# Performance work log

Hardware: AMD Instinct MI355X
Metric: run time of the kernel (lower is better)

## Reference

```python
import jax, jax.numpy as jnp
import numpy as np
from functools import partial

VOCAB, D, H, L, T_MAX = 32000, 1024, 16, 8, 1024
HD = D // H
HIDDEN = int(D * 2.67)  # 2734, matches int(n_embd*hidden_mult)


def setup_inputs() -> dict:
    key = jax.random.key(0)
    ks = jax.random.split(key, 9)
    s = 0.02
    return {
        "idx": jax.random.randint(ks[0], (2, 1024), 0, VOCAB),
        "W_emb": jax.random.normal(ks[1], (VOCAB, D), jnp.float32) * s,  # tied with lm_head
        "norm1_w": jnp.ones((L, D), jnp.float32),
        "Wqkv": jax.random.normal(ks[2], (L, D, 3 * D), jnp.float32) * s,
        "Wout": jax.random.normal(ks[3], (L, D, D), jnp.float32) * s,
        "norm2_w": jnp.ones((L, D), jnp.float32),
        "Wg": jax.random.normal(ks[4], (L, D, HIDDEN), jnp.float32) * s,
        "Wu": jax.random.normal(ks[5], (L, D, HIDDEN), jnp.float32) * s,
        "Wd": jax.random.normal(ks[6], (L, HIDDEN, D), jnp.float32) * s,
        "final_norm_w": jnp.ones((D,), jnp.float32),
    }


def _rmsnorm(x, w, eps=1e-6):
    rms = jnp.sqrt(jnp.mean(x * x, axis=-1, keepdims=True) + eps)
    return x / rms * w


def _rope(x, cos_f, sin_f):
    # x: [B,H,T,hd]; cos_f/sin_f: [T, hd//2]
    x1, x2 = x[..., : HD // 2], x[..., HD // 2 :]
    c = cos_f[None, None]
    s = sin_f[None, None]
    return jnp.concatenate([x1 * c - x2 * s, x1 * s + x2 * c], axis=-1)


def _forward(idx, W_emb, norm1_w, Wqkv, Wout, norm2_w, Wg, Wu, Wd, final_norm_w):
    B, T = idx.shape
    # RoPE tables (buffers in the torch module)
    inv_freq = 1.0 / (10000.0 ** (jnp.arange(0, HD, 2, dtype=jnp.float32) / HD))
    ang = jnp.arange(T, dtype=jnp.float32)[:, None] * inv_freq[None, :]  # [T, hd//2]
    cos_f, sin_f = jnp.cos(ang), jnp.sin(ang)
    causal = jnp.tril(jnp.ones((T, T), dtype=bool))  # [T,T]
    scale = 1.0 / jnp.sqrt(jnp.float32(HD))

    def block(x, params):
        n1, wqkv, wout, n2, wg, wu, wd = params
        h = _rmsnorm(x, n1)
        qkv = (h @ wqkv).reshape(B, T, 3, H, HD).transpose(2, 0, 3, 1, 4)  # [3,B,H,T,hd]
        q, k, v = qkv[0], qkv[1], qkv[2]
        q = _rope(q, cos_f, sin_f)
        k = _rope(k, cos_f, sin_f)
        attn = jnp.einsum("bhqd,bhkd->bhqk", q, k) * scale
        attn = jnp.where(causal[None, None], attn, -jnp.inf)
        attn = jax.nn.softmax(attn, axis=-1)
        o = jnp.einsum("bhqk,bhkd->bhqd", attn, v)
        o = o.transpose(0, 2, 1, 3).reshape(B, T, D) @ wout
        x = x + o
        h2 = _rmsnorm(x, n2)
        x = x + (jax.nn.silu(h2 @ wg) * (h2 @ wu)) @ wd
        return x, None

    x = W_emb[idx]  # [B,T,D]
    x, _ = jax.lax.scan(block, x, (norm1_w, Wqkv, Wout, norm2_w, Wg, Wu, Wd))
    x = _rmsnorm(x, final_norm_w)
    return x @ W_emb.T  # tied lm_head -> [B,T,VOCAB]


def reference(idx, W_emb, norm1_w, Wqkv, Wout, norm2_w, Wg, Wu, Wd, final_norm_w):
    return _forward(idx, W_emb, norm1_w, Wqkv, Wout, norm2_w, Wg, Wu, Wd, final_norm_w)
```

## Files before the change

kernel.cpp:

```cpp
#include <hip/hip_runtime.h>
#include <cstdint>
#include <cmath>

#define D_MODEL 1024
#define T_SEQ   1024
#define NHEAD   16
#define NLAYER  8
#define HID     2734
#define HID_PAD 2816
#define NTOK    2048
#define VOCAB   32000

typedef __bf16 bf16x8 __attribute__((ext_vector_type(8)));
typedef __bf16 bf16x4 __attribute__((ext_vector_type(4)));
typedef float  f32x4  __attribute__((ext_vector_type(4)));

__device__ inline bf16x4 to_bf4(float a, float b, float c, float d) {
  bf16x4 t; t[0] = (__bf16)a; t[1] = (__bf16)b; t[2] = (__bf16)c; t[3] = (__bf16)d; return t;
}

__device__ inline void gload16(const __bf16* g, __bf16* l) {
  __builtin_amdgcn_global_load_lds(
      (const __attribute__((address_space(1))) void*)g,
      (__attribute__((address_space(3))) void*)l, 16, 0, 0);
}

__global__ __launch_bounds__(256) void embed_kernel(const int* __restrict__ idx,
                                                    const float* __restrict__ W,
                                                    float* __restrict__ x) {
  int t = blockIdx.x;
  int v = idx[t];
  float4 val = *(const float4*)&W[(size_t)v * D_MODEL + threadIdx.x * 4];
  *(float4*)&x[(size_t)t * D_MODEL + threadIdx.x * 4] = val;
}

__global__ __launch_bounds__(256) void rmsnorm_kernel(const float* __restrict__ x,
                                                      const float* __restrict__ w,
                                                      __bf16* __restrict__ out) {
  int row = blockIdx.x;
  int tid = threadIdx.x;
  float4 v = *(const float4*)&x[(size_t)row * D_MODEL + tid * 4];
  float s = v.x * v.x + v.y * v.y + v.z * v.z + v.w * v.w;
#pragma unroll
  for (int m = 32; m >= 1; m >>= 1) s += __shfl_xor(s, m, 64);
  __shared__ float red[4];
  if ((tid & 63) == 0) red[tid >> 6] = s;
  __syncthreads();
  float tot = red[0] + red[1] + red[2] + red[3];
  float inv = rsqrtf(tot * (1.0f / (float)D_MODEL) + 1e-6f);
  float4 wv = *(const float4*)&w[tid * 4];
  bf16x4 o4 = to_bf4(v.x * inv * wv.x, v.y * inv * wv.y, v.z * inv * wv.z, v.w * inv * wv.w);
  *(bf16x4*)&out[(size_t)row * D_MODEL + tid * 4] = o4;
}

__global__ __launch_bounds__(256) void rope_table_kernel(float* __restrict__ tab) {
  int p = blockIdx.x * 256 + threadIdx.x;
  int t = p >> 5, i = p & 31;
  float freq = exp2f(-(float)i * (13.287712379549449f / 32.0f));
  float sn, cs;
  sincosf((float)t * freq, &sn, &cs);
  tab[p] = cs;
  tab[32768 + p] = sn;
}

__global__ __launch_bounds__(256) void tp5_kernel(
    const float* __restrict__ Wqkv, const float* __restrict__ Wout,
    const float* __restrict__ Wg, const float* __restrict__ Wu,
    const float* __restrict__ Wd,
    __bf16* __restrict__ wqkvT, __bf16* __restrict__ woutT,
    __bf16* __restrict__ wguT, __bf16* __restrict__ wdT) {
  __shared__ __bf16 tile[64][65];
  int t = blockIdx.x;
  const float* in;
  __bf16* out;
  int R, C, Ro, rmul, roff, tr;
  if (t < 768)        { in = Wqkv; out = wqkvT; R = 1024; C = 3072; Ro = 1024; rmul = 1; roff = 0; tr = 16; }
  else if (t < 1024)  { t -= 768;  in = Wout; out = woutT; R = 1024; C = 1024; Ro = 1024; rmul = 1; roff = 0; tr = 16; }
  else if (t < 1728)  { t -= 1024; in = Wg; out = wguT; R = 1024; C = HID; Ro = 1024; rmul = 2; roff = 0; tr = 16; }
  else if (t < 2432)  { t -= 1728; in = Wu; out = wguT; R = 1024; C = HID; Ro = 1024; rmul = 2; roff = 1; tr = 16; }
  else                { t -= 2432; in = Wd; out = wdT; R = HID; C = 1024; Ro = HID_PAD; rmul = 1; roff = 0; tr = 44; }
  int r0 = (t % tr) * 64, c0 = (t / tr) * 64;
  int tid = threadIdx.x;
  bool fullc = (c0 + 64 <= C);
#pragma unroll
  for (int i = 0; i < 4; ++i) {
    int ri = i * 16 + (tid >> 4);
    int ci = (tid & 15) * 4;
    int r = r0 + ri;
    float4 v = {0.f, 0.f, 0.f, 0.f};
    if (r < R) {
      const float* p = in + (size_t)r * C + c0 + ci;
      if (fullc) {
        v = *(const float4*)p;
      } else {
        int c = c0 + ci;
        if (c + 0 < C) v.x = p[0];
        if (c + 1 < C) v.y = p[1];
        if (c + 2 < C) v.z = p[2];
        if (c + 3 < C) v.w = p[3];
      }
    }
    tile[ri][ci + 0] = (__bf16)v.x;
    tile[ri][ci + 1] = (__bf16)v.y;
    tile[ri][ci + 2] = (__bf16)v.z;
    tile[ri][ci + 3] = (__bf16)v.w;
  }
  __syncthreads();
#pragma unroll
  for (int i = 0; i < 4; ++i) {
    int oc = i * 16 + (tid >> 4);
    int orr = (tid & 15) * 4;
    bf16x4 tv;
    tv[0] = tile[orr + 0][oc];
    tv[1] = tile[orr + 1][oc];
    tv[2] = tile[orr + 2][oc];
    tv[3] = tile[orr + 3][oc];
    *(bf16x4*)&out[((size_t)(c0 + oc) * rmul + roff) * Ro + r0 + orr] = tv;
  }
}

__global__ __launch_bounds__(256) void convert_bf16_kernel(const float* __restrict__ in,
                                                           __bf16* __restrict__ out, int n4) {
  for (int i = blockIdx.x * 256 + threadIdx.x; i < n4; i += gridDim.x * 256) {
    float4 v = ((const float4*)in)[i];
    ((bf16x4*)out)[i] = to_bf4(v.x, v.y, v.z, v.w);
  }
}

template <int BM, int BN, int WM, int WN, int EPI>
__global__ __launch_bounds__(WM * WN * 64, 2) void gemm8(
    const __bf16* __restrict__ A, const __bf16* __restrict__ B,
    const float* __restrict__ Cin, void* __restrict__ Cout,
    int K, int ldc,
    const float* __restrict__ Tab, __bf16* __restrict__ Qr,
    __bf16* __restrict__ Kr, __bf16* __restrict__ Vt) {
  constexpr int NTH = WM * WN * 64;
  constexpr int MF = BM / (16 * WM);
  constexpr int MG = (MF + 3) / 4;
  constexpr int CL = (MF < 4) ? MF : 4;
  constexpr int LA = (BM * 4) / NTH;
  constexpr int LB = (BN * 4) / NTH;
  static_assert(BN / WN == 64, "NF must be 4");
  __shared__ __align__(16) __bf16 lds[(BM + BN) * 128];

  const int tid = threadIdx.x;
  const int lane = tid & 63, wid = tid >> 6;
  const int wr = wid / WN, wn = wid % WN;
  const int lr = lane & 15, lg = lane >> 4;

  const int gx = gridDim.x;
  const int nwg = gx * gridDim.y;
  const int orig = blockIdx.y * gx + blockIdx.x;
  const int q = nwg >> 3, r8 = nwg & 7;
  const int xcd = orig & 7, loc = orig >> 3;
  const int swz = ((xcd < r8) ? xcd * (q + 1) : r8 * (q + 1) + (xcd - r8) * q) + loc;
  const int brow = (swz % gx) * BM;
  const int bcol = (swz / gx) * BN;

  const __bf16* pAg[LA];
  const __bf16* pBg[LB];
  int opA[LA], opB[LB];
#pragma unroll
  for (int i = 0; i < LA; ++i) {
    int p = tid + i * NTH;
    int row = ((p >> 6) << 4) | (p & 15), j = (p >> 4) & 3;
    pAg[i] = A + (size_t)(brow + row) * K + j * 8;
    opA[i] = p * 8;
  }
#pragma unroll
  for (int i = 0; i < LB; ++i) {
    int p = tid + i * NTH;
    int row = ((p >> 6) << 4) | (p & 15), j = (p >> 4) & 3;
    pBg[i] = B + (size_t)(bcol + row) * K + j * 8;
    opB[i] = p * 8;
  }

  const int ntiles = K >> 6;

  auto STAGE_A = [&](int v, int kkq) {
    int vs = v < ntiles ? v : ntiles - 1;
    int ko = vs * 64 + kkq * 32;
    int sa = (v & 1) * (BM * 64) + kkq * (BM * 32);
#pragma unroll
    for (int i = 0; i < LA; ++i) gload16(pAg[i] + ko, lds + sa + opA[i]);
  };
  auto STAGE_B = [&](int v, int kkq) {
    int vs = v < ntiles ? v : ntiles - 1;
    int ko = vs * 64 + kkq * 32;
    int sb = BM * 128 + (v & 1) * (BN * 64) + kkq * (BN * 32);
#pragma unroll
    for (int i = 0; i < LB; ++i) gload16(pBg[i] + ko, lds + sb + opB[i]);
  };

  f32x4 acc[MF][4];
#pragma unroll
  for (int m = 0; m < MF; ++m)
#pragma unroll
    for (int n = 0; n < 4; ++n) acc[m][n] = (f32x4){0.f, 0.f, 0.f, 0.f};

  STAGE_A(0, 0); STAGE_B(0, 0);
  STAGE_A(0, 1); STAGE_B(0, 1);
  STAGE_A(1, 0); STAGE_B(1, 0);

  const int fragoff = lg * 128 + lr * 8;

  if constexpr (MF == 8) {
    for (int u = 0; u < ntiles; ++u) {
      const int buf = u & 1;
#pragma unroll
      for (int kk = 0; kk < 2; ++kk) {
        const int v = (kk == 0) ? u + 1 : u + 2;
        const int kkq = kk ^ 1;
        const __bf16* Ab = lds + buf * (BM * 64) + kk * (BM * 32);
        const __bf16* Bb = lds + BM * 128 + buf * (BN * 64) + kk * (BN * 32);
        asm volatile("s_waitcnt vmcnt(8)" ::: "memory");
        __builtin_amdgcn_sched_barrier(0);
        __builtin_amdgcn_s_barrier();
        __builtin_amdgcn_sched_barrier(0);
        STAGE_A(v, kkq);
        bf16x8 bfr[4], af0[4];
#pragma unroll
        for (int n = 0; n < 4; ++n)
          bfr[n] = *(const bf16x8*)(Bb + (wn * 64 + n * 16) * 32 + fragoff);
#pragma unroll
        for (int i = 0; i < 4; ++i)
          af0[i] = *(const bf16x8*)(Ab + (wr * 128 + i * 16) * 32 + fragoff);
        asm volatile("s_waitcnt lgkmcnt(0)" ::: "memory");
        __builtin_amdgcn_sched_barrier(0);
        __builtin_amdgcn_s_setprio(1);
#pragma unroll
        for (int i = 0; i < 4; ++i)
#pragma unroll
          for (int n = 0; n < 4; ++n)
            acc[i][n] = __builtin_amdgcn_mfma_f32_16x16x32_bf16(af0[i], bfr[n], acc[i][n], 0, 0, 0);
        __builtin_amdgcn_s_setprio(0);
        __builtin_amdgcn_s_barrier();
        STAGE_B(v, kkq);
        bf16x8 af1[4];
#pragma unroll
        for (int i = 0; i < 4; ++i)
          af1[i] = *(const bf16x8*)(Ab + (wr * 128 + 64 + i * 16) * 32 + fragoff);
        asm volatile("s_waitcnt lgkmcnt(0)" ::: "memory");
        __builtin_amdgcn_sched_barrier(0);
        __builtin_amdgcn_s_setprio(1);
#pragma unroll
        for (int i = 0; i < 4; ++i)
#pragma unroll
          for (int n = 0; n < 4; ++n)
            acc[4 + i][n] = __builtin_amdgcn_mfma_f32_16x16x32_bf16(af1[i], bfr[n], acc[4 + i][n], 0, 0, 0);
        __builtin_amdgcn_s_setprio(0);
        __builtin_amdgcn_s_barrier();
      }
    }
  } else {
    for (int u = 0; u < ntiles; ++u) {
      const int buf = u & 1;
#pragma unroll
      for (int kk = 0; kk < 2; ++kk) {
        if constexpr (LA + LB == 3) asm volatile("s_waitcnt vmcnt(6)" ::: "memory");
        else                        asm volatile("s_waitcnt vmcnt(8)" ::: "memory");
        __builtin_amdgcn_sched_barrier(0);
        __builtin_amdgcn_s_barrier();
        __builtin_amdgcn_sched_barrier(0);
        const int v = (kk == 0) ? u + 1 : u + 2;
        const int kkq = kk ^ 1;
        STAGE_A(v, kkq);
        STAGE_B(v, kkq);
        const __bf16* Ab = lds + buf * (BM * 64) + kk * (BM * 32);
        const __bf16* Bb = lds + BM * 128 + buf * (BN * 64) + kk * (BN * 32);
        bf16x8 bfr[4];
#pragma unroll
        for (int n = 0; n < 4; ++n)
          bfr[n] = *(const bf16x8*)(Bb + (wn * 64 + n * 16) * 32 + fragoff);
#pragma unroll
        for (int mg = 0; mg < MG; ++mg) {
          bf16x8 afr[CL];
#pragma unroll
          for (int i = 0; i < CL; ++i)
            afr[i] = *(const bf16x8*)(Ab + (wr * (BM / WM) + (mg * 4 + i) * 16) * 32 + fragoff);
          __builtin_amdgcn_s_setprio(1);
#pragma unroll
          for (int i = 0; i < CL; ++i)
#pragma unroll
            for (int n = 0; n < 4; ++n)
              acc[mg * 4 + i][n] =
                  __builtin_amdgcn_mfma_f32_16x16x32_bf16(afr[i], bfr[n], acc[mg * 4 + i][n], 0, 0, 0);
          __builtin_amdgcn_s_setprio(0);
        }
      }
    }
  }

  if constexpr (EPI == 5) {
    const int colw = bcol + wn * 64;
    const int secw = colw >> 10;
    const int h = (colw >> 6) & 15;
#pragma unroll
    for (int m = 0; m < MF; ++m) {
      int row0 = brow + wr * (BM / WM) + m * 16 + lg * 4;
      int bb = row0 >> 10;
      int t0 = row0 & 1023;
      int bh = bb * 16 + h;
      if (secw < 2) {
        __bf16* base = (secw == 0 ? Qr : Kr) + ((size_t)bh * T_SEQ + t0) * 64;
#pragma unroll
        for (int n = 0; n < 2; ++n) {
          int din = n * 16 + lr;
#pragma unroll
          for (int rr = 0; rr < 4; ++rr) {
            float a = acc[m][n][rr], b2 = acc[m][n + 2][rr];
            float cs = Tab[(t0 + rr) * 32 + din];
            float sn = Tab[32768 + (t0 + rr) * 32 + din];
            base[(size_t)rr * 64 + din]      = (__bf16)(a * cs - b2 * sn);
            base[(size_t)rr * 64 + din + 32] = (__bf16)(a * sn + b2 * cs);
          }
        }
      } else {
#pragma unroll
        for (int n = 0; n < 4; ++n) {
          int din = n * 16 + lr;
          bf16x4 pk;
#pragma unroll
          for (int rr = 0; rr < 4; ++rr) pk[rr] = (__bf16)acc[m][n][rr];
          *(bf16x4*)&Vt[((size_t)bh * 64 + din) * T_SEQ + t0] = pk;
        }
      }
    }
  } else {
#pragma unroll
    for (int m = 0; m < MF; ++m) {
#pragma unroll
      for (int n = 0; n < 4; ++n) {
#pragma unroll
        for (int rr = 0; rr < 4; ++rr) {
          int row = brow + wr * (BM / WM) + m * 16 + lg * 4 + rr;
          int col = bcol + wn * 64 + n * 16 + lr;
          size_t off = (size_t)row * ldc + col;
          float vv = acc[m][n][rr];
          if (EPI == 0) {
            ((float*)Cout)[off] = vv;
          } else if (EPI == 1) {
            ((float*)Cout)[off] = Cin[off] + vv;
          } else {
            float uv = __shfl_xor(vv, 1);
            if ((lr & 1) == 0) {
              float r = vv / (1.f + __expf(-vv)) * uv;
              ((__bf16*)Cout)[(size_t)row * ldc + (col >> 1)] = (__bf16)r;
            }
          }
        }
      }
    }
  }
}

__global__ __launch_bounds__(256) void attn_kernel(const __bf16* __restrict__ Qr,
                                                   const __bf16* __restrict__ Kr,
                                                   const __bf16* __restrict__ Vt,
                                                   __bf16* __restrict__ o) {
  __shared__ __align__(16) __bf16 lds[28672];
  const int tid = threadIdx.x;
  const int lane = tid & 63, w = tid >> 6;
  const int lr = lane & 15, lg = lane >> 4;
  const int bh = blockIdx.y, b = bh >> 4, h = bh & 15;
  const int qp = blockIdx.x;
  const __bf16* Kg = Kr + (size_t)bh * T_SEQ * 64;
  const __bf16* Vg = Vt + (size_t)bh * 64 * T_SEQ;
  const float scale = 0.125f;
  __bf16* Pw = lds + 20480 + w * 2048;

  for (int qs = 0; qs < 2; ++qs) {
    const int qb = qs ? (15 - qp) : qp;
    const int q0 = qb * 64;
    const __bf16* Qg = Qr + ((size_t)bh * T_SEQ + q0) * 64;

    __syncthreads();
    {
      int row = ((tid >> 6) << 4) | (tid & 15);
      int j = (tid >> 4) & 3;
      gload16(Qg + row * 64 + j * 8, lds + tid * 8);
      gload16(Qg + row * 64 + 32 + j * 8, lds + 2048 + tid * 8);
    }

    f32x4 accO[4];
#pragma unroll
    for (int n = 0; n < 4; ++n) accO[n] = (f32x4){0.f, 0.f, 0.f, 0.f};
    float mrow[4], lrow[4];
#pragma unroll
    for (int r = 0; r < 4; ++r) { mrow[r] = -1e30f; lrow[r] = 0.f; }

    const int ntile = ((q0 + 63) >> 7) + 1;

    for (int tt = 0; tt < ntile; ++tt) {
      const int j0 = tt * 128;
      __syncthreads();
#pragma unroll
      for (int i = 0; i < 2; ++i) {
        int p = tid + i * 256;
        int row = ((p >> 6) << 4) | (p & 15), j = (p >> 4) & 3;
        const __bf16* src = Kg + (size_t)(j0 + row) * 64 + j * 8;
        gload16(src, lds + 4096 + p * 8);
        gload16(src + 32, lds + 8192 + p * 8);
      }
#pragma unroll
      for (int s = 0; s < 4; ++s) {
        int d = ((tid >> 6) << 4) | (tid & 15), j = (tid >> 4) & 3;
        gload16(Vg + (size_t)d * T_SEQ + j0 + s * 32 + j * 8, lds + 12288 + s * 2048 + tid * 8);
      }
      __syncthreads();

      f32x4 s4[8];
#pragma unroll
      for (int n = 0; n < 8; ++n) s4[n] = (f32x4){0.f, 0.f, 0.f, 0.f};
#pragma unroll
      for (int kk = 0; kk < 2; ++kk) {
        bf16x8 aq = *(const bf16x8*)(lds + kk * 2048 + (w * 64 + lg * 16 + lr) * 8);
        __builtin_amdgcn_s_setprio(1);
#pragma unroll
        for (int jf = 0; jf < 8; ++jf) {
          bf16x8 bk = *(const bf16x8*)(lds + 4096 + kk * 4096 + (jf * 64 + lg * 16 + lr) * 8);
          s4[jf] = __builtin_amdgcn_mfma_f32_16x16x32_bf16(aq, bk, s4[jf], 0, 0, 0);
        }
        __builtin_amdgcn_s_setprio(0);
      }

      float pm[4];
#pragma unroll
      for (int r = 0; r < 4; ++r) pm[r] = -1e30f;
#pragma unroll
      for (int jf = 0; jf < 8; ++jf) {
        int gj = j0 + jf * 16 + lr;
#pragma unroll
        for (int r = 0; r < 4; ++r) {
          int gq = q0 + w * 16 + lg * 4 + r;
          float sv = s4[jf][r] * scale;
          if (gj > gq) sv = -1e30f;
          s4[jf][r] = sv;
          pm[r] = fmaxf(pm[r], sv);
        }
      }
#pragma unroll
      for (int r = 0; r < 4; ++r) {
#pragma unroll
        for (int m = 8; m >= 1; m >>= 1) pm[r] = fmaxf(pm[r], __shfl_xor(pm[r], m, 64));
      }
      float alpha[4];
#pragma unroll
      for (int r = 0; r < 4; ++r) {
        float mn = fmaxf(mrow[r], pm[r]);
        alpha[r] = expf(mrow[r] - mn);
        mrow[r] = mn;
      }
      float ps[4] = {0.f, 0.f, 0.f, 0.f};
#pragma unroll
      for (int jf = 0; jf < 8; ++jf) {
#pragma unroll
        for (int r = 0; r < 4; ++r) {
          float p = expf(s4[jf][r] - mrow[r]);
          s4[jf][r] = p;
          ps[r] += p;
        }
      }
#pragma unroll
      for (int r = 0; r < 4; ++r) {
#pragma unroll
        for (int m = 8; m >= 1; m >>= 1) ps[r] += __shfl_xor(ps[r], m, 64);
        lrow[r] = lrow[r] * alpha[r] + ps[r];
      }
#pragma unroll
      for (int n = 0; n < 4; ++n) {
#pragma unroll
        for (int r = 0; r < 4; ++r) accO[n][r] *= alpha[r];
      }

#pragma unroll
      for (int jf = 0; jf < 8; ++jf) {
        int s = jf >> 1;
        int rem = ((jf & 1) << 4) + lr;
        int base = s * 512 + (rem >> 3) * 128 + (rem & 7);
#pragma unroll
        for (int r = 0; r < 4; ++r) {
          int qloc = lg * 4 + r;
          Pw[base + qloc * 8] = (__bf16)s4[jf][r];
        }
      }
      asm volatile("s_waitcnt lgkmcnt(0)" ::: "memory");
      __builtin_amdgcn_sched_barrier(0);

#pragma unroll
      for (int s = 0; s < 4; ++s) {
        bf16x8 pa = *(const bf16x8*)(Pw + s * 512 + (lg * 16 + lr) * 8);
        __builtin_amdgcn_s_setprio(1);
#pragma unroll
        for (int nd = 0; nd < 4; ++nd) {
          bf16x8 bv = *(const bf16x8*)(lds + 12288 + s * 2048 + (nd * 64 + lg * 16 + lr) * 8);
          accO[nd] = __builtin_amdgcn_mfma_f32_16x16x32_bf16(pa, bv, accO[nd], 0, 0, 0);
        }
        __builtin_amdgcn_s_setprio(0);
      }
    }

#pragma unroll
    for (int nd = 0; nd < 4; ++nd) {
#pragma unroll
      for (int r = 0; r < 4; ++r) {
        int gq = q0 + w * 16 + lg * 4 + r;
        float val = accO[nd][r] / lrow[r];
        o[(size_t)(b * T_SEQ + gq) * D_MODEL + h * 64 + nd * 16 + lr] = (__bf16)val;
      }
    }
  }
}

extern "C" void kernel_launch(void* const* d_in, const int* in_sizes, int n_in,
                              void* d_out, int out_size, void* d_ws, size_t ws_size,
                              hipStream_t stream) {
  const int*   idx     = (const int*)d_in[0];
  const float* W_emb   = (const float*)d_in[1];
  const float* norm1_w = (const float*)d_in[2];
  const float* Wqkv    = (const float*)d_in[3];
  const float* Wout    = (const float*)d_in[4];
  const float* norm2_w = (const float*)d_in[5];
  const float* Wg      = (const float*)d_in[6];
  const float* Wu      = (const float*)d_in[7];
  const float* Wd      = (const float*)d_in[8];
  const float* fnorm   = (const float*)d_in[9];
  float* out = (float*)d_out;

  float*  x    = (float*)d_ws;
  float*  tab  = x + (size_t)NTOK * D_MODEL;
  __bf16* hb   = (__bf16*)(tab + 2 * 32768);
  __bf16* ob   = hb + (size_t)NTOK * D_MODEL;
  __bf16* ga   = ob + (size_t)NTOK * D_MODEL;
  __bf16* Qrb  = ga + (size_t)NTOK * HID_PAD;
  __bf16* Krb  = Qrb + (size_t)32 * T_SEQ * 64;
  __bf16* Vtb  = Krb + (size_t)32 * T_SEQ * 64;
  __bf16* wbuf = Vtb + (size_t)32 * T_SEQ * 64;

  __bf16* wqkvT = wbuf;
  __bf16* woutT = wqkvT + (size_t)3 * D_MODEL * D_MODEL;
  __bf16* wguT  = woutT + (size_t)D_MODEL * D_MODEL;
  __bf16* wdT   = wguT + (size_t)2 * HID_PAD * D_MODEL;

  embed_kernel<<<NTOK, 256, 0, stream>>>(idx, W_emb, x);
  rope_table_kernel<<<128, 256, 0, stream>>>(tab);

  for (int l = 0; l < NLAYER; ++l) {
    tp5_kernel<<<3136, 256, 0, stream>>>(
        Wqkv + (size_t)l * D_MODEL * 3 * D_MODEL,
        Wout + (size_t)l * D_MODEL * D_MODEL,
        Wg + (size_t)l * D_MODEL * HID,
        Wu + (size_t)l * D_MODEL * HID,
        Wd + (size_t)l * HID * D_MODEL,
        wqkvT, woutT, wguT, wdT);

    rmsnorm_kernel<<<NTOK, 256, 0, stream>>>(x, norm1_w + (size_t)l * D_MODEL, hb);
    gemm8<128, 256, 2, 4, 5><<<dim3(16, 12), 512, 0, stream>>>(
        hb, wqkvT, nullptr, nullptr, D_MODEL, 3 * D_MODEL, tab, Qrb, Krb, Vtb);
    attn_kernel<<<dim3(8, 32), 256, 0, stream>>>(Qrb, Krb, Vtb, ob);
    gemm8<128, 64, 4, 1, 1><<<dim3(16, 16), 256, 0, stream>>>(
        ob, woutT, x, x, D_MODEL, D_MODEL, nullptr, nullptr, nullptr, nullptr);
    rmsnorm_kernel<<<NTOK, 256, 0, stream>>>(x, norm2_w + (size_t)l * D_MODEL, hb);
    gemm8<256, 256, 2, 4, 4><<<dim3(8, 22), 512, 0, stream>>>(
        hb, wguT, nullptr, ga, D_MODEL, HID_PAD, nullptr, nullptr, nullptr, nullptr);
    gemm8<128, 64, 4, 1, 1><<<dim3(16, 16), 256, 0, stream>>>(
        ga, wdT, x, x, HID_PAD, D_MODEL, nullptr, nullptr, nullptr, nullptr);
  }

  rmsnorm_kernel<<<NTOK, 256, 0, stream>>>(x, fnorm, hb);
  convert_bf16_kernel<<<2048, 256, 0, stream>>>(W_emb, wbuf, VOCAB * D_MODEL / 4);
  gemm8<256, 256, 2, 4, 0><<<dim3(8, 125), 512, 0, stream>>>(
      hb, wbuf, nullptr, out, D_MODEL, VOCAB, nullptr, nullptr, nullptr, nullptr);
}
```

Measured before the change: 1.734 ms.

## Batch weight transposes, fuse embed/rope, split attention blocks, retile gate-up GEMM

When the workspace is large enough, the weights of all layers are transposed to bf16 in one large launch instead of one launch per layer. The embedding gather and RoPE table build are merged into a single kernel. Attention now gives each query block its own workgroup (512 blocks with launch_bounds 2), where before each workgroup handled a balanced pair of query blocks. The gate/up GEMM uses a 128-row tile so it launches twice as many workgroups. The cost is a larger workspace footprint and possible load imbalance in attention.

```diff
diff --git a/kernel.cpp b/kernel.cpp
--- a/kernel.cpp
+++ b/kernel.cpp
@@ -11,6 +11,12 @@
 #define NTOK    2048
 #define VOCAB   32000
 
+#define WQKV_EL  (3072 * 1024)
+#define WOUT_EL  (1024 * 1024)
+#define WGU_EL   (2 * 2816 * 1024)
+#define WD_EL    (1024 * 2816)
+#define LW_EL    (WQKV_EL + WOUT_EL + WGU_EL + WD_EL)
+
 typedef __bf16 bf16x8 __attribute__((ext_vector_type(8)));
 typedef __bf16 bf16x4 __attribute__((ext_vector_type(4)));
 typedef float  f32x4  __attribute__((ext_vector_type(4)));
@@ -25,13 +31,24 @@
       (__attribute__((address_space(3))) void*)l, 16, 0, 0);
 }
 
-__global__ __launch_bounds__(256) void embed_kernel(const int* __restrict__ idx,
-                                                    const float* __restrict__ W,
-                                                    float* __restrict__ x) {
-  int t = blockIdx.x;
-  int v = idx[t];
-  float4 val = *(const float4*)&W[(size_t)v * D_MODEL + threadIdx.x * 4];
-  *(float4*)&x[(size_t)t * D_MODEL + threadIdx.x * 4] = val;
+__global__ __launch_bounds__(256) void embed_rope_kernel(const int* __restrict__ idx,
+                                                         const float* __restrict__ W,
+                                                         float* __restrict__ x,
+                                                         float* __restrict__ tab) {
+  int blk = blockIdx.x;
+  if (blk < NTOK) {
+    int v = idx[blk];
+    float4 val = *(const float4*)&W[(size_t)v * D_MODEL + threadIdx.x * 4];
+    *(float4*)&x[(size_t)blk * D_MODEL + threadIdx.x * 4] = val;
+  } else {
+    int p = (blk - NTOK) * 256 + threadIdx.x;
+    int t = p >> 5, i = p & 31;
+    float freq = exp2f(-(float)i * (13.287712379549449f / 32.0f));
+    float sn, cs;
+    sincosf((float)t * freq, &sn, &cs);
+    tab[p] = cs;
+    tab[32768 + p] = sn;
+  }
 }
 
 __global__ __launch_bounds__(256) void rmsnorm_kernel(const float* __restrict__ x,
@@ -53,32 +70,29 @@
   *(bf16x4*)&out[(size_t)row * D_MODEL + tid * 4] = o4;
 }
 
-__global__ __launch_bounds__(256) void rope_table_kernel(float* __restrict__ tab) {
-  int p = blockIdx.x * 256 + threadIdx.x;
-  int t = p >> 5, i = p & 31;
-  float freq = exp2f(-(float)i * (13.287712379549449f / 32.0f));
-  float sn, cs;
-  sincosf((float)t * freq, &sn, &cs);
-  tab[p] = cs;
-  tab[32768 + p] = sn;
-}
-
 __global__ __launch_bounds__(256) void tp5_kernel(
     const float* __restrict__ Wqkv, const float* __restrict__ Wout,
     const float* __restrict__ Wg, const float* __restrict__ Wu,
-    const float* __restrict__ Wd,
-    __bf16* __restrict__ wqkvT, __bf16* __restrict__ woutT,
-    __bf16* __restrict__ wguT, __bf16* __restrict__ wdT) {
+    const float* __restrict__ Wd, __bf16* __restrict__ wAll,
+    int l0, int dstMult) {
   __shared__ __bf16 tile[64][65];
-  int t = blockIdx.x;
+  int bl = blockIdx.x / 3136;
+  int t  = blockIdx.x % 3136;
+  int ll = l0 + bl;
+  size_t dbase = (size_t)(dstMult ? ll : 0) * LW_EL;
+  __bf16* wqkvT = wAll + dbase;
+  __bf16* woutT = wqkvT + WQKV_EL;
+  __bf16* wguT  = woutT + WOUT_EL;
+  __bf16* wdT   = wguT + WGU_EL;
+
   const float* in;
   __bf16* out;
   int R, C, Ro, rmul, roff, tr;
-  if (t < 768)        { in = Wqkv; out = wqkvT; R = 1024; C = 3072; Ro = 1024; rmul = 1; roff = 0; tr = 16; }
-  else if (t < 1024)  { t -= 768;  in = Wout; out = woutT; R = 1024; C = 1024; Ro = 1024; rmul = 1; roff = 0; tr = 16; }
-  else if (t < 1728)  { t -= 1024; in = Wg; out = wguT; R = 1024; C = HID; Ro = 1024; rmul = 2; roff = 0; tr = 16; }
-  else if (t < 2432)  { t -= 1728; in = Wu; out = wguT; R = 1024; C = HID; Ro = 1024; rmul = 2; roff = 1; tr = 16; }
-  else                { t -= 2432; in = Wd; out = wdT; R = HID; C = 1024; Ro = HID_PAD; rmul = 1; roff = 0; tr = 44; }
+  if (t < 768)        { in = Wqkv + (size_t)ll * 1024 * 3072; out = wqkvT; R = 1024; C = 3072; Ro = 1024; rmul = 1; roff = 0; tr = 16; }
+  else if (t < 1024)  { t -= 768;  in = Wout + (size_t)ll * 1024 * 1024; out = woutT; R = 1024; C = 1024; Ro = 1024; rmul = 1; roff = 0; tr = 16; }
+  else if (t < 1728)  { t -= 1024; in = Wg + (size_t)ll * 1024 * HID; out = wguT; R = 1024; C = HID; Ro = 1024; rmul = 2; roff = 0; tr = 16; }
+  else if (t < 2432)  { t -= 1728; in = Wu + (size_t)ll * 1024 * HID; out = wguT; R = 1024; C = HID; Ro = 1024; rmul = 2; roff = 1; tr = 16; }
+  else                { t -= 2432; in = Wd + (size_t)ll * HID * 1024; out = wdT; R = HID; C = 1024; Ro = HID_PAD; rmul = 1; roff = 0; tr = 44; }
   int r0 = (t % tr) * 64, c0 = (t / tr) * 64;
   int tid = threadIdx.x;
   bool fullc = (c0 + 64 <= C);
@@ -354,160 +368,156 @@
   }
 }
 
-__global__ __launch_bounds__(256) void attn_kernel(const __bf16* __restrict__ Qr,
-                                                   const __bf16* __restrict__ Kr,
-                                                   const __bf16* __restrict__ Vt,
-                                                   __bf16* __restrict__ o) {
+__global__ __launch_bounds__(256, 2) void attn_kernel(const __bf16* __restrict__ Qr,
+                                                      const __bf16* __restrict__ Kr,
+                                                      const __bf16* __restrict__ Vt,
+                                                      __bf16* __restrict__ o) {
   __shared__ __align__(16) __bf16 lds[28672];
   const int tid = threadIdx.x;
   const int lane = tid & 63, w = tid >> 6;
   const int lr = lane & 15, lg = lane >> 4;
-  const int bh = blockIdx.y, b = bh >> 4, h = bh & 15;
-  const int qp = blockIdx.x;
+  const int L = blockIdx.x;
+  const int qb = (L < 256) ? (L >> 5) : 15 - ((L - 256) >> 5);
+  const int bh = L & 31, b = bh >> 4, h = bh & 15;
+  const int q0 = qb * 64;
+  const __bf16* Qg = Qr + ((size_t)bh * T_SEQ + q0) * 64;
   const __bf16* Kg = Kr + (size_t)bh * T_SEQ * 64;
   const __bf16* Vg = Vt + (size_t)bh * 64 * T_SEQ;
   const float scale = 0.125f;
   __bf16* Pw = lds + 20480 + w * 2048;
 
-  for (int qs = 0; qs < 2; ++qs) {
-    const int qb = qs ? (15 - qp) : qp;
-    const int q0 = qb * 64;
-    const __bf16* Qg = Qr + ((size_t)bh * T_SEQ + q0) * 64;
-
+  {
+    int row = ((tid >> 6) << 4) | (tid & 15);
+    int j = (tid >> 4) & 3;
+    gload16(Qg + row * 64 + j * 8, lds + tid * 8);
+    gload16(Qg + row * 64 + 32 + j * 8, lds + 2048 + tid * 8);
+  }
+
+  f32x4 accO[4];
+#pragma unroll
+  for (int n = 0; n < 4; ++n) accO[n] = (f32x4){0.f, 0.f, 0.f, 0.f};
+  float mrow[4], lrow[4];
+#pragma unroll
+  for (int r = 0; r < 4; ++r) { mrow[r] = -1e30f; lrow[r] = 0.f; }
+
+  const int ntile = (qb >> 1) + 1;
+
+  for (int tt = 0; tt < ntile; ++tt) {
+    const int j0 = tt * 128;
     __syncthreads();
-    {
-      int row = ((tid >> 6) << 4) | (tid & 15);
-      int j = (tid >> 4) & 3;
-      gload16(Qg + row * 64 + j * 8, lds + tid * 8);
-      gload16(Qg + row * 64 + 32 + j * 8, lds + 2048 + tid * 8);
-    }
-
-    f32x4 accO[4];
-#pragma unroll
-    for (int n = 0; n < 4; ++n) accO[n] = (f32x4){0.f, 0.f, 0.f, 0.f};
-    float mrow[4], lrow[4];
-#pragma unroll
-    for (int r = 0; r < 4; ++r) { mrow[r] = -1e30f; lrow[r] = 0.f; }
-
-    const int ntile = ((q0 + 63) >> 7) + 1;
-
-    for (int tt = 0; tt < ntile; ++tt) {
-      const int j0 = tt * 128;
-      __syncthreads();
-#pragma unroll
-      for (int i = 0; i < 2; ++i) {
-        int p = tid + i * 256;
-        int row = ((p >> 6) << 4) | (p & 15), j = (p >> 4) & 3;
-        const __bf16* src = Kg + (size_t)(j0 + row) * 64 + j * 8;
-        gload16(src, lds + 4096 + p * 8);
-        gload16(src + 32, lds + 8192 + p * 8);
-      }
-#pragma unroll
-      for (int s = 0; s < 4; ++s) {
-        int d = ((tid >> 6) << 4) | (tid & 15), j = (tid >> 4) & 3;
-        gload16(Vg + (size_t)d * T_SEQ + j0 + s * 32 + j * 8, lds + 12288 + s * 2048 + tid * 8);
-      }
-      __syncthreads();
-
-      f32x4 s4[8];
-#pragma unroll
-      for (int n = 0; n < 8; ++n) s4[n] = (f32x4){0.f, 0.f, 0.f, 0.f};
-#pragma unroll
-      for (int kk = 0; kk < 2; ++kk) {
-        bf16x8 aq = *(const bf16x8*)(lds + kk * 2048 + (w * 64 + lg * 16 + lr) * 8);
-        __builtin_amdgcn_s_setprio(1);
-#pragma unroll
-        for (int jf = 0; jf < 8; ++jf) {
-          bf16x8 bk = *(const bf16x8*)(lds + 4096 + kk * 4096 + (jf * 64 + lg * 16 + lr) * 8);
-          s4[jf] = __builtin_amdgcn_mfma_f32_16x16x32_bf16(aq, bk, s4[jf], 0, 0, 0);
-        }
-        __builtin_amdgcn_s_setprio(0);
-      }
-
-      float pm[4];
-#pragma unroll
-      for (int r = 0; r < 4; ++r) pm[r] = -1e30f;
+#pragma unroll
+    for (int i = 0; i < 2; ++i) {
+      int p = tid + i * 256;
+      int row = ((p >> 6) << 4) | (p & 15), j = (p >> 4) & 3;
+      const __bf16* src = Kg + (size_t)(j0 + row) * 64 + j * 8;
+      gload16(src, lds + 4096 + p * 8);
+      gload16(src + 32, lds + 8192 + p * 8);
+    }
+#pragma unroll
+    for (int s = 0; s < 4; ++s) {
+      int d = ((tid >> 6) << 4) | (tid & 15), j = (tid >> 4) & 3;
+      gload16(Vg + (size_t)d * T_SEQ + j0 + s * 32 + j * 8, lds + 12288 + s * 2048 + tid * 8);
+    }
+    __syncthreads();
+
+    f32x4 s4[8];
+#pragma unroll
+    for (int n = 0; n < 8; ++n) s4[n] = (f32x4){0.f, 0.f, 0.f, 0.f};
+#pragma unroll
+    for (int kk = 0; kk < 2; ++kk) {
+      bf16x8 aq = *(const bf16x8*)(lds + kk * 2048 + (w * 64 + lg * 16 + lr) * 8);
+      __builtin_amdgcn_s_setprio(1);
 #pragma unroll
       for (int jf = 0; jf < 8; ++jf) {
-        int gj = j0 + jf * 16 + lr;
-#pragma unroll
-        for (int r = 0; r < 4; ++r) {
-          int gq = q0 + w * 16 + lg * 4 + r;
-          float sv = s4[jf][r] * scale;
-          if (gj > gq) sv = -1e30f;
-          s4[jf][r] = sv;
-          pm[r] = fmaxf(pm[r], sv);
-        }
-      }
-#pragma unroll
-      for (int r = 0; r < 4; ++r) {
-#pragma unroll
-        for (int m = 8; m >= 1; m >>= 1) pm[r] = fmaxf(pm[r], __shfl_xor(pm[r], m, 64));
-      }
-      float alpha[4];
-#pragma unroll
-      for (int r = 0; r < 4; ++r) {
-        float mn = fmaxf(mrow[r], pm[r]);
-        alpha[r] = expf(mrow[r] - mn);
-        mrow[r] = mn;
-      }
-      float ps[4] = {0.f, 0.f, 0.f, 0.f};
-#pragma unroll
-      for (int jf = 0; jf < 8; ++jf) {
-#pragma unroll
-        for (int r = 0; r < 4; ++r) {
-          float p = expf(s4[jf][r] - mrow[r]);
-          s4[jf][r] = p;
-          ps[r] += p;
-        }
-      }
-#pragma unroll
-      for (int r = 0; r < 4; ++r) {
-#pragma unroll
-        for (int m = 8; m >= 1; m >>= 1) ps[r] += __shfl_xor(ps[r], m, 64);
-        lrow[r] = lrow[r] * alpha[r] + ps[r];
-      }
-#pragma unroll
-      for (int n = 0; n < 4; ++n) {
-#pragma unroll
-        for (int r = 0; r < 4; ++r) accO[n][r] *= alpha[r];
-      }
-
-#pragma unroll
-      for (int jf = 0; jf < 8; ++jf) {
-        int s = jf >> 1;
-        int rem = ((jf & 1) << 4) + lr;
-        int base = s * 512 + (rem >> 3) * 128 + (rem & 7);
-#pragma unroll
-        for (int r = 0; r < 4; ++r) {
-          int qloc = lg * 4 + r;
-          Pw[base + qloc * 8] = (__bf16)s4[jf][r];
-        }
-      }
-      asm volatile("s_waitcnt lgkmcnt(0)" ::: "memory");
-      __builtin_amdgcn_sched_barrier(0);
-
-#pragma unroll
-      for (int s = 0; s < 4; ++s) {
-        bf16x8 pa = *(const bf16x8*)(Pw + s * 512 + (lg * 16 + lr) * 8);
-        __builtin_amdgcn_s_setprio(1);
-#pragma unroll
-        for (int nd = 0; nd < 4; ++nd) {
-          bf16x8 bv = *(const bf16x8*)(lds + 12288 + s * 2048 + (nd * 64 + lg * 16 + lr) * 8);
-          accO[nd] = __builtin_amdgcn_mfma_f32_16x16x32_bf16(pa, bv, accO[nd], 0, 0, 0);
-        }
-        __builtin_amdgcn_s_setprio(0);
-      }
-    }
-
-#pragma unroll
-    for (int nd = 0; nd < 4; ++nd) {
+        bf16x8 bk = *(const bf16x8*)(lds + 4096 + kk * 4096 + (jf * 64 + lg * 16 + lr) * 8);
+        s4[jf] = __builtin_amdgcn_mfma_f32_16x16x32_bf16(aq, bk, s4[jf], 0, 0, 0);
+      }
+      __builtin_amdgcn_s_setprio(0);
+    }
+
+    float pm[4];
+#pragma unroll
+    for (int r = 0; r < 4; ++r) pm[r] = -1e30f;
+#pragma unroll
+    for (int jf = 0; jf < 8; ++jf) {
+      int gj = j0 + jf * 16 + lr;
 #pragma unroll
       for (int r = 0; r < 4; ++r) {
         int gq = q0 + w * 16 + lg * 4 + r;
-        float val = accO[nd][r] / lrow[r];
-        o[(size_t)(b * T_SEQ + gq) * D_MODEL + h * 64 + nd * 16 + lr] = (__bf16)val;
-      }
+        float sv = s4[jf][r] * scale;
+        if (gj > gq) sv = -1e30f;
+        s4[jf][r] = sv;
+        pm[r] = fmaxf(pm[r], sv);
+      }
+    }
+#pragma unroll
+    for (int r = 0; r < 4; ++r) {
+#pragma unroll
+      for (int m = 8; m >= 1; m >>= 1) pm[r] = fmaxf(pm[r], __shfl_xor(pm[r], m, 64));
+    }
+    float alpha[4];
+#pragma unroll
+    for (int r = 0; r < 4; ++r) {
+      float mn = fmaxf(mrow[r], pm[r]);
+      alpha[r] = expf(mrow[r] - mn);
+      mrow[r] = mn;
+    }
+    float ps[4] = {0.f, 0.f, 0.f, 0.f};
+#pragma unroll
+    for (int jf = 0; jf < 8; ++jf) {
+#pragma unroll
+      for (int r = 0; r < 4; ++r) {
+        float p = expf(s4[jf][r] - mrow[r]);
+        s4[jf][r] = p;
+        ps[r] += p;
+      }
+    }
+#pragma unroll
+    for (int r = 0; r < 4; ++r) {
+#pragma unroll
+      for (int m = 8; m >= 1; m >>= 1) ps[r] += __shfl_xor(ps[r], m, 64);
+      lrow[r] = lrow[r] * alpha[r] + ps[r];
+    }
+#pragma unroll
+    for (int n = 0; n < 4; ++n) {
+#pragma unroll
+      for (int r = 0; r < 4; ++r) accO[n][r] *= alpha[r];
+    }
+
+#pragma unroll
+    for (int jf = 0; jf < 8; ++jf) {
+      int s = jf >> 1;
+      int rem = ((jf & 1) << 4) + lr;
+      int base = s * 512 + (rem >> 3) * 128 + (rem & 7);
+#pragma unroll
+      for (int r = 0; r < 4; ++r) {
+        int qloc = lg * 4 + r;
+        Pw[base + qloc * 8] = (__bf16)s4[jf][r];
+      }
+    }
+    asm volatile("s_waitcnt lgkmcnt(0)" ::: "memory");
+    __builtin_amdgcn_sched_barrier(0);
+
+#pragma unroll
+    for (int s = 0; s < 4; ++s) {
+      bf16x8 pa = *(const bf16x8*)(Pw + s * 512 + (lg * 16 + lr) * 8);
+      __builtin_amdgcn_s_setprio(1);
+#pragma unroll
+      for (int nd = 0; nd < 4; ++nd) {
+        bf16x8 bv = *(const bf16x8*)(lds + 12288 + s * 2048 + (nd * 64 + lg * 16 + lr) * 8);
+        accO[nd] = __builtin_amdgcn_mfma_f32_16x16x32_bf16(pa, bv, accO[nd], 0, 0, 0);
+      }
+      __builtin_amdgcn_s_setprio(0);
+    }
+  }
+
+#pragma unroll
+  for (int nd = 0; nd < 4; ++nd) {
+#pragma unroll
+    for (int r = 0; r < 4; ++r) {
+      int gq = q0 + w * 16 + lg * 4 + r;
+      float val = accO[nd][r] / lrow[r];
+      o[(size_t)(b * T_SEQ + gq) * D_MODEL + h * 64 + nd * 16 + lr] = (__bf16)val;
     }
   }
 }
@@ -535,40 +545,44 @@
   __bf16* Qrb  = ga + (size_t)NTOK * HID_PAD;
   __bf16* Krb  = Qrb + (size_t)32 * T_SEQ * 64;
   __bf16* Vtb  = Krb + (size_t)32 * T_SEQ * 64;
-  __bf16* wbuf = Vtb + (size_t)32 * T_SEQ * 64;
-
-  __bf16* wqkvT = wbuf;
-  __bf16* woutT = wqkvT + (size_t)3 * D_MODEL * D_MODEL;
-  __bf16* wguT  = woutT + (size_t)D_MODEL * D_MODEL;
-  __bf16* wdT   = wguT + (size_t)2 * HID_PAD * D_MODEL;
-
-  embed_kernel<<<NTOK, 256, 0, stream>>>(idx, W_emb, x);
-  rope_table_kernel<<<128, 256, 0, stream>>>(tab);
+  __bf16* wAll = Vtb + (size_t)32 * T_SEQ * 64;
+
+  size_t headB = ((size_t)NTOK * D_MODEL + 2 * 32768) * 4 +
+                 ((size_t)NTOK * D_MODEL * 3 + (size_t)NTOK * HID_PAD +
+                  (size_t)3 * 32 * T_SEQ * 64) * 2;
+  bool allmode = ws_size >= headB + (size_t)NLAYER * LW_EL * 2;
+
+  embed_rope_kernel<<<NTOK + 128, 256, 0, stream>>>(idx, W_emb, x, tab);
+
+  if (allmode) {
+    tp5_kernel<<<3136 * NLAYER, 256, 0, stream>>>(Wqkv, Wout, Wg, Wu, Wd, wAll, 0, 1);
+  }
 
   for (int l = 0; l < NLAYER; ++l) {
-    tp5_kernel<<<3136, 256, 0, stream>>>(
-        Wqkv + (size_t)l * D_MODEL * 3 * D_MODEL,
-        Wout + (size_t)l * D_MODEL * D_MODEL,
-        Wg + (size_t)l * D_MODEL * HID,
-        Wu + (size_t)l * D_MODEL * HID,
-        Wd + (size_t)l * HID * D_MODEL,
-        wqkvT, woutT, wguT, wdT);
+    if (!allmode) {
+      tp5_kernel<<<3136, 256, 0, stream>>>(Wqkv, Wout, Wg, Wu, Wd, wAll, l, 0);
+    }
+    __bf16* wL = wAll + (allmode ? (size_t)l * LW_EL : 0);
+    __bf16* wqkvT = wL;
+    __bf16* woutT = wqkvT + WQKV_EL;
+    __bf16* wguT  = woutT + WOUT_EL;
+    __bf16* wdT   = wguT + WGU_EL;
 
     rmsnorm_kernel<<<NTOK, 256, 0, stream>>>(x, norm1_w + (size_t)l * D_MODEL, hb);
     gemm8<128, 256, 2, 4, 5><<<dim3(16, 12), 512, 0, stream>>>(
         hb, wqkvT, nullptr, nullptr, D_MODEL, 3 * D_MODEL, tab, Qrb, Krb, Vtb);
-    attn_kernel<<<dim3(8, 32), 256, 0, stream>>>(Qrb, Krb, Vtb, ob);
+    attn_kernel<<<512, 256, 0, stream>>>(Qrb, Krb, Vtb, ob);
     gemm8<128, 64, 4, 1, 1><<<dim3(16, 16), 256, 0, stream>>>(
         ob, woutT, x, x, D_MODEL, D_MODEL, nullptr, nullptr, nullptr, nullptr);
     rmsnorm_kernel<<<NTOK, 256, 0, stream>>>(x, norm2_w + (size_t)l * D_MODEL, hb);
-    gemm8<256, 256, 2, 4, 4><<<dim3(8, 22), 512, 0, stream>>>(
+    gemm8<128, 256, 2, 4, 4><<<dim3(16, 22), 512, 0, stream>>>(
         hb, wguT, nullptr, ga, D_MODEL, HID_PAD, nullptr, nullptr, nullptr, nullptr);
     gemm8<128, 64, 4, 1, 1><<<dim3(16, 16), 256, 0, stream>>>(
         ga, wdT, x, x, HID_PAD, D_MODEL, nullptr, nullptr, nullptr, nullptr);
   }
 
   rmsnorm_kernel<<<NTOK, 256, 0, stream>>>(x, fnorm, hb);
-  convert_bf16_kernel<<<2048, 256, 0, stream>>>(W_emb, wbuf, VOCAB * D_MODEL / 4);
+  convert_bf16_kernel<<<2048, 256, 0, stream>>>(W_emb, wAll, VOCAB * D_MODEL / 4);
   gemm8<256, 256, 2, 4, 0><<<dim3(8, 125), 512, 0, stream>>>(
-      hb, wbuf, nullptr, out, D_MODEL, VOCAB, nullptr, nullptr, nullptr, nullptr);
-}
+      hb, wAll, nullptr, out, D_MODEL, VOCAB, nullptr, nullptr, nullptr, nullptr);
+}
```

Measured after the change: 1.854 ms. 1.07x slower.
